# Optimization experiments

Measured on AMD Instinct MI355X. Metric: run time of the kernel, lower is better.

Reference implementation:

```python
import jax, jax.numpy as jnp
import numpy as np

N, E, C, H, T, R = 32768, 262144, 128, 8, 8, 8
DK = C // H


def _typed_linear(feat, W, b, tid):
    # per-type linear: rows with tid==t get feat @ W[t] + b[t]; others untouched base 0
    out = jnp.zeros((feat.shape[0], W.shape[-1]), feat.dtype)
    for t in range(W.shape[0]):
        m = (tid == t)[:, None]
        out = jnp.where(m, feat @ W[t] + b[t], out)
    return out


def _forward(x, type_id, edge_index, edge_attr, Wk, bk, Wq, bq, Wv, bv, Wa, ba,
             relation_pri, relation_att, relation_msg, skip, gamma, beta):
    n, c = x.shape
    r, h, dk, _ = relation_att.shape
    src, dst = edge_index[0], edge_index[1]
    fs, fd = x[src], x[dst]                      # [E, C] gathers
    # per-edge-type k/q/v projections (source masks by edge_attr)
    k = _typed_linear(fs, Wk, bk, edge_attr).reshape(-1, h, dk)
    q = _typed_linear(fd, Wq, bq, edge_attr).reshape(-1, h, dk)
    v = _typed_linear(fs, Wv, bv, edge_attr).reshape(-1, h, dk)
    # relation transforms without materializing [E,h,dk,dk] gathers
    kt = jnp.zeros_like(k)
    vt = jnp.zeros_like(v)
    for ri in range(r):
        m = (edge_attr == ri)[:, None, None]
        kt = jnp.where(m, jnp.einsum('ehd,hdk->ehk', k, relation_att[ri]), kt)
        vt = jnp.where(m, jnp.einsum('ehd,hdk->ehk', v, relation_msg[ri]), vt)
    pri = relation_pri[edge_attr]                # [E, H]
    att = (q * kt).sum(-1) * pri / jnp.sqrt(jnp.asarray(dk, x.dtype))  # [E, H]
    # scatter softmax over destination-node groups
    mx = jax.ops.segment_max(att, dst, num_segments=n)
    ex = jnp.exp(att - mx[dst])
    den = jax.ops.segment_sum(ex, dst, num_segments=n)
    a = ex / den[dst]                            # [E, H]
    w = (a[..., None] * vt).reshape(-1, h * dk)  # [E, C]
    # scatter mean into node slots (zeros for isolated nodes)
    s = jax.ops.segment_sum(w, dst, num_segments=n)
    cnt = jax.ops.segment_sum(jnp.ones((w.shape[0], 1), x.dtype), dst, num_segments=n)
    x0 = jnp.where(cnt > 0, s / jnp.maximum(cnt, 1.0), 0.0)
    # per-node-type output projection + gated residual
    x0 = _typed_linear(x0, Wa, ba, type_id)
    alpha = jax.nn.sigmoid(skip)[type_id][:, None]
    out = x0 * alpha + x * (1.0 - alpha)
    # type-indexed LayerNorm (eps = 1e-5), dropout is identity in eval
    mu = out.mean(-1, keepdims=True)
    var = ((out - mu) ** 2).mean(-1, keepdims=True)
    xn = (out - mu) / jnp.sqrt(var + 1e-5)
    return xn * gamma[type_id] + beta[type_id]


def setup_inputs() -> dict:
    key = jax.random.key(0)
    ks = jax.random.split(key, 16)
    w = 1.0 / np.sqrt(C)
    wr = 1.0 / np.sqrt(DK)
    return {
        'x': jax.random.normal(ks[0], (N, C), jnp.float32),
        'type_id': jax.random.randint(ks[1], (N,), 0, T),
        'edge_index': jax.random.randint(ks[2], (2, E), 0, N),
        'edge_attr': jax.random.randint(ks[3], (E,), 0, R),
        'Wk': jax.random.normal(ks[4], (T, C, C), jnp.float32) * w,
        'bk': jax.random.normal(ks[5], (T, C), jnp.float32) * 0.02,
        'Wq': jax.random.normal(ks[6], (T, C, C), jnp.float32) * w,
        'bq': jax.random.normal(ks[7], (T, C), jnp.float32) * 0.02,
        'Wv': jax.random.normal(ks[8], (T, C, C), jnp.float32) * w,
        'bv': jax.random.normal(ks[9], (T, C), jnp.float32) * 0.02,
        'Wa': jax.random.normal(ks[10], (T, C, C), jnp.float32) * w,
        'ba': jax.random.normal(ks[11], (T, C), jnp.float32) * 0.02,
        'relation_pri': jnp.ones((R, H), jnp.float32),
        'relation_att': jax.random.normal(ks[12], (R, H, DK, DK), jnp.float32) * wr,
        'relation_msg': jax.random.normal(ks[13], (R, H, DK, DK), jnp.float32) * wr,
        'skip': jnp.ones((T,), jnp.float32),
        'gamma': jnp.ones((T, C), jnp.float32),
        'beta': jnp.zeros((T, C), jnp.float32),
    }


def reference(x, type_id, edge_index, edge_attr, Wk, bk, Wq, bq, Wv, bv, Wa, ba,
              relation_pri, relation_att, relation_msg, skip, gamma, beta):
    return _forward(x, type_id, edge_index, edge_attr, Wk, bk, Wq, bq, Wv, bv, Wa, ba,
                    relation_pri, relation_att, relation_msg, skip, gamma, beta)
```

## Files before the change

kernel.cpp:

```cpp
#include <hip/hip_runtime.h>
#include <math.h>

#define NN 32768
#define NE 262144
#define CD 128
#define NH 8
#define NT 8
#define NR 8

typedef unsigned short u16;
typedef unsigned long long ull;
typedef __attribute__((ext_vector_type(8))) short bhalf8;
typedef __attribute__((ext_vector_type(4))) float f32x4;


__device__ __forceinline__ u16 f2b(float f) {
    union { float f; unsigned u; } v; v.f = f;
    unsigned r = v.u + 0x7FFF + ((v.u >> 16) & 1);
    return (u16)(r >> 16);
}
__device__ __forceinline__ float b2f(unsigned h) {
    union { unsigned u; float f; } v; v.u = h << 16;
    return v.f;
}

#define PREP_BLOCKS 2057
#define ZB_BLOCKS 256
#define XB_BLOCKS 2048

__global__ void prep_zero(const float* __restrict__ Wk, const float* __restrict__ bk,
                          const float* __restrict__ Wq,
                          const float* __restrict__ Wv, const float* __restrict__ bv,
                          const float* __restrict__ Wa,
                          const float* __restrict__ Aatt, const float* __restrict__ Amsg,
                          const float* __restrict__ x,
                          u16* __restrict__ WqT, u16* __restrict__ WkT,
                          u16* __restrict__ WvT, u16* __restrict__ WaT,
                          float* __restrict__ bkf, float* __restrict__ bvf,
                          int* __restrict__ degd, u16* __restrict__ xb) {
    if (blockIdx.x >= PREP_BLOCKS + ZB_BLOCKS) {
        int zi = (blockIdx.x - PREP_BLOCKS - ZB_BLOCKS) * 256 + threadIdx.x;
        long basei = (long)zi * 8;
        float4 v0 = *(const float4*)(x + basei);
        float4 v1 = *(const float4*)(x + basei + 4);
        bhalf8 pk;
        pk[0] = (short)f2b(v0.x); pk[1] = (short)f2b(v0.y);
        pk[2] = (short)f2b(v0.z); pk[3] = (short)f2b(v0.w);
        pk[4] = (short)f2b(v1.x); pk[5] = (short)f2b(v1.y);
        pk[6] = (short)f2b(v1.z); pk[7] = (short)f2b(v1.w);
        *(bhalf8*)(xb + basei) = pk;
        return;
    }
    if (blockIdx.x >= PREP_BLOCKS) {
        int zi = (blockIdx.x - PREP_BLOCKS) * 256 + threadIdx.x;
        if (zi < 2 * NN) degd[zi] = 0;
        return;
    }
    const int WCNT = NT * CD * CD;
    int idx = blockIdx.x * 256 + threadIdx.x;
    if (idx < 4 * WCNT) {
        int mat = idx >> 17;
        int o = idx & (WCNT - 1);
        int t = o >> 14;
        int n = (o >> 7) & 127;
        int k = o & 127;
        int ct = n >> 4, lx2 = n & 15, kk = k >> 5, qd = (k >> 3) & 3, dd = k & 7;
        int oo = t * 16384 + (((ct * 4 + kk) * 4 + qd) * 16 + lx2) * 8 + dd;
        if (mat == 0) {
            WqT[oo] = f2b(Wq[(t * CD + k) * CD + n]);
        } else if (mat == 3) {
            WaT[oo] = f2b(Wa[(t * CD + k) * CD + n]);
        } else {
            int h = n >> 4, j = n & 15;
            const float* W = (mat == 1) ? Wk : Wv;
            const float* A = (mat == 1) ? Aatt : Amsg;
            const float* wrow = W + (t * CD + k) * CD + h * 16;
            const float* acol = A + ((t * NH + h) * 16) * 16 + j;
            float s = 0.f;
#pragma unroll
            for (int d = 0; d < 16; ++d) s += wrow[d] * acol[d * 16];
            ((mat == 1) ? WkT : WvT)[oo] = f2b(s);
        }
    } else {
        int o2 = idx - 4 * WCNT;
        if (o2 < 2 * NT * CD) {
            int which = (o2 >= NT * CD) ? 1 : 0;
            int o = o2 - which * NT * CD;
            const float* B = which ? bv : bk;
            const float* A = which ? Amsg : Aatt;
            int t = o >> 7; int c = o & 127; int h = c >> 4; int j = c & 15;
            const float* brow = B + t * CD + h * 16;
            const float* acol = A + ((t * NH + h) * 16) * 16 + j;
            float s = 0.f;
#pragma unroll
            for (int d = 0; d < 16; ++d) s += brow[d] * acol[d * 16];
            (which ? bvf : bkf)[o] = s;
        }
    }
}

__global__ void hists(const int* __restrict__ ea, const int* __restrict__ tidv,
                      const int* __restrict__ dstv,
                      int* __restrict__ epart, int* __restrict__ npart,
                      int* __restrict__ deg) {
    __shared__ int wc[4][8];
    const int b = blockIdx.x;
    const int tid = threadIdx.x;
    const int lane = tid & 63, w = tid >> 6;
    int i = b * 256 + tid;
    int t = ea[i];
    atomicAdd(&deg[dstv[i]], 1);
#pragma unroll
    for (int u = 0; u < 8; ++u) {
        ull m = __ballot(t == u);
        if (lane == 0) wc[w][u] = __popcll(m);
    }
    __syncthreads();
    if (tid < 8) epart[b * 8 + tid] = wc[0][tid] + wc[1][tid] + wc[2][tid] + wc[3][tid];
    if (b < NN / 256) {
        int tn = tidv[i];
        __syncthreads();
#pragma unroll
        for (int u = 0; u < 8; ++u) {
            ull m = __ballot(tn == u);
            if (lane == 0) wc[w][u] = __popcll(m);
        }
        __syncthreads();
        if (tid < 8) npart[b * 8 + tid] = wc[0][tid] + wc[1][tid] + wc[2][tid] + wc[3][tid];
    }
}

__launch_bounds__(1024)
__global__ void scan_all(const int* __restrict__ deg, int* __restrict__ dbase,
                         int* __restrict__ epart, int* __restrict__ npart,
                         int* __restrict__ ectr, int* __restrict__ nctr) {
    const int t = threadIdx.x;
    if (blockIdx.x == 0) {
        __shared__ int part[1024];
        int local[32];
        int s = 0;
#pragma unroll
        for (int i = 0; i < 32; ++i) { local[i] = s; s += deg[t * 32 + i]; }
        part[t] = s;
        __syncthreads();
        for (int off = 1; off < 1024; off <<= 1) {
            int v = (t >= off) ? part[t - off] : 0;
            __syncthreads();
            part[t] += v;
            __syncthreads();
        }
        int base = (t == 0) ? 0 : part[t - 1];
#pragma unroll
        for (int i = 0; i < 32; ++i) dbase[t * 32 + i] = base + local[i];
        return;
    }
    __shared__ int sc[1024 * 8];
    int v[8], orig[8];
#pragma unroll
    for (int u = 0; u < 8; ++u) { orig[u] = v[u] = epart[t * 8 + u]; sc[t * 8 + u] = v[u]; }
    for (int off = 1; off < 1024; off <<= 1) {
        __syncthreads();
        int wv[8];
        bool p = (t >= off);
        if (p) {
#pragma unroll
            for (int u = 0; u < 8; ++u) wv[u] = sc[(t - off) * 8 + u];
        }
        __syncthreads();
        if (p) {
#pragma unroll
            for (int u = 0; u < 8; ++u) { v[u] += wv[u]; sc[t * 8 + u] = v[u]; }
        }
    }
    __syncthreads();
    int tot[8], base[8];
    {
        int acc = 0;
#pragma unroll
        for (int u = 0; u < 8; ++u) { tot[u] = sc[1023 * 8 + u]; base[u] = acc; acc += tot[u]; }
    }
#pragma unroll
    for (int u = 0; u < 8; ++u) epart[t * 8 + u] = base[u] + v[u] - orig[u];
    if (t == 0) {
        ectr[8] = 0; ectr[17] = 0;
        int acc = 0, ptb = 0;
        for (int u = 0; u < 8; ++u) {
            acc += tot[u]; ectr[9 + u] = acc;
            ptb += (tot[u] + 63) >> 6; ectr[18 + u] = ptb;
        }
    }
    __syncthreads();
    int nv[8], nor[8];
#pragma unroll
    for (int u = 0; u < 8; ++u) {
        nor[u] = nv[u] = (t < 128) ? npart[t * 8 + u] : 0;
        sc[t * 8 + u] = nv[u];
    }
    for (int off = 1; off < 128; off <<= 1) {
        __syncthreads();
        int wv[8];
        bool p = (t >= off && t < 128);
        if (p) {
#pragma unroll
            for (int u = 0; u < 8; ++u) wv[u] = sc[(t - off) * 8 + u];
        }
        __syncthreads();
        if (p) {
#pragma unroll
            for (int u = 0; u < 8; ++u) { nv[u] += wv[u]; sc[t * 8 + u] = nv[u]; }
        }
    }
    __syncthreads();
    int ntot[8], nbase[8];
    {
        int acc = 0;
#pragma unroll
        for (int u = 0; u < 8; ++u) { ntot[u] = sc[127 * 8 + u]; nbase[u] = acc; acc += ntot[u]; }
    }
    if (t < 128) {
#pragma unroll
        for (int u = 0; u < 8; ++u) npart[t * 8 + u] = nbase[u] + nv[u] - nor[u];
    }
    if (t == 0) {
        nctr[8] = 0; nctr[17] = 0;
        int acc = 0, ptb = 0;
        for (int u = 0; u < 8; ++u) {
            acc += ntot[u]; nctr[9 + u] = acc;
            ptb += (ntot[u] + 63) >> 6; nctr[18 + u] = ptb;
        }
    }
}

__global__ void scatter2(const int* __restrict__ ea, const int* __restrict__ tidv,
                         const int* __restrict__ srcv, const int* __restrict__ dstv,
                         const int* __restrict__ epart, const int* __restrict__ npart,
                         const int* __restrict__ dbase, int* __restrict__ dcur,
                         int4* __restrict__ epack, int* __restrict__ nperm) {
    __shared__ int wc[4][8];
    __shared__ int wo[4][8];
    const int b = blockIdx.x;
    const int tid = threadIdx.x;
    const int lane = tid & 63, w = tid >> 6;
    const bool is_e = (b < NE / 256);
    const int* lab; const int* off; int i;
    if (is_e) { lab = ea; off = epart + b * 8; i = b * 256 + tid; }
    else { lab = tidv; off = npart + (b - NE / 256) * 8; i = (b - NE / 256) * 256 + tid; }
    int t = lab[i];
    const ull below = (1ull << lane) - 1;
    int myrank = 0;
#pragma unroll
    for (int u = 0; u < 8; ++u) {
        ull m = __ballot(t == u);
        if (lane == 0) wc[w][u] = __popcll(m);
        if (t == u) myrank = __popcll(m & below);
    }
    __syncthreads();
    if (tid < 32) {
        int u = tid & 7, w2 = tid >> 3;
        int s = 0;
        for (int w3 = 0; w3 < w2; ++w3) s += wc[w3][u];
        wo[w2][u] = s;
    }
    __syncthreads();
    int slot = off[t] + wo[w][t] + myrank;
    if (is_e) {
        int s = srcv[i], d = dstv[i];
        int pos = dbase[d] + atomicAdd(&dcur[d], 1);
        epack[slot] = int4{s, d, pos, 0};
    } else {
        nperm[slot] = i;
    }
}

__device__ __forceinline__ void gemm64g(const u16* __restrict__ sA,
                                        const u16* __restrict__ gW,
                                        int rh, int ch, int lx, int quad, int lane,
                                        const float* __restrict__ biasRow,
                                        f32x4 acc[2][4]) {
#pragma unroll
    for (int nt = 0; nt < 4; ++nt) {
        float bv = biasRow[ch * 64 + nt * 16 + lx];
        acc[0][nt] = f32x4{bv, bv, bv, bv};
        acc[1][nt] = f32x4{bv, bv, bv, bv};
    }
    const int m0 = rh * 32 + lx;
    const u16* wbase = gW + (ch * 4) * 2048 + lane * 8;
    bhalf8 bb[2][4];
#pragma unroll
    for (int nt = 0; nt < 4; ++nt)
        bb[0][nt] = *(const bhalf8*)(wbase + nt * 2048);
#pragma unroll
    for (int kk = 0; kk < 4; ++kk) {
        if (kk < 3) {
#pragma unroll
            for (int nt = 0; nt < 4; ++nt)
                bb[(kk + 1) & 1][nt] = *(const bhalf8*)(wbase + nt * 2048 + (kk + 1) * 512);
        }
        const int ko = kk * 32 + quad * 8;
        bhalf8 a0 = *(const bhalf8*)&sA[m0 * 136 + ko];
        bhalf8 a1 = *(const bhalf8*)&sA[(m0 + 16) * 136 + ko];
#pragma unroll
        for (int nt = 0; nt < 4; ++nt) {
            acc[0][nt] = __builtin_amdgcn_mfma_f32_16x16x32_bf16(a0, bb[kk & 1][nt], acc[0][nt], 0, 0, 0);
            acc[1][nt] = __builtin_amdgcn_mfma_f32_16x16x32_bf16(a1, bb[kk & 1][nt], acc[1][nt], 0, 0, 0);
        }
    }
}

__launch_bounds__(256, 4)
__global__ void edge_kernel(const u16* __restrict__ xb,
                            const u16* __restrict__ WqT, const float* __restrict__ bq,
                            const u16* __restrict__ WkT, const float* __restrict__ bkf,
                            const u16* __restrict__ WvT, const float* __restrict__ bvf,
                            const float* __restrict__ pri,
                            const int* __restrict__ ectr, const int4* __restrict__ epack,
                            float* __restrict__ exs, u16* __restrict__ vts) {
    __shared__ u16 sFS[64 * 136];
    __shared__ u16 sFD[64 * 136];
    __shared__ int sSrc[64], sDst[64], sPos[64];

    const int tid = threadIdx.x;
    const int lane = tid & 63;
    const int w = tid >> 6;
    const int lx = lane & 15;
    const int quad = lane >> 4;
    const int ch = w & 1;
    const int rh = w >> 1;
    const int b = blockIdx.x;

    int t = -1, lt = 0;
#pragma unroll
    for (int u = 0; u < NR; ++u) {
        int p0 = ectr[17 + u], p1 = ectr[18 + u];
        if (b >= p0 && b < p1) { t = u; lt = b - p0; }
    }
    if (t < 0) return;
    const int base = ectr[8 + t];
    const int sz = ectr[9 + t] - base;
    const int start = lt * 64;

    if (tid < 64) {
        int idx = start + tid;
        int4 pk = (idx < sz) ? epack[base + idx] : int4{0, 0, NE, 0};
        sSrc[tid] = pk.x;
        sDst[tid] = pk.y;
        sPos[tid] = pk.z;
    }
    __syncthreads();

#pragma unroll
    for (int it = 0; it < 4; ++it) {
        int c = tid + it * 256;
        int row = c >> 4, off = (c & 15) * 8;
        *(bhalf8*)&sFS[row * 136 + off] = *(const bhalf8*)&xb[(long)sSrc[row] * CD + off];
        *(bhalf8*)&sFD[row * 136 + off] = *(const bhalf8*)&xb[(long)sDst[row] * CD + off];
    }
    __syncthreads();

    f32x4 qa[2][4], ka[2][4];
    gemm64g(sFD, WqT + t * 16384, rh, ch, lx, quad, lane, bq + t * CD, qa);
    gemm64g(sFS, WkT + t * 16384, rh, ch, lx, quad, lane, bkf + t * CD, ka);

    float ex[2][4][4];
#pragma unroll
    for (int nt = 0; nt < 4; ++nt) {
        const float ph = pri[t * NH + ch * 4 + nt] * 0.25f;
#pragma unroll
        for (int mt = 0; mt < 2; ++mt) {
#pragma unroll
            for (int reg = 0; reg < 4; ++reg) {
                float p = qa[mt][nt][reg] * ka[mt][nt][reg];
                p += __shfl_xor(p, 1);
                p += __shfl_xor(p, 2);
                p += __shfl_xor(p, 4);
                p += __shfl_xor(p, 8);
                ex[mt][nt][reg] = __expf(p * ph);
            }
        }
    }
    if (lx == 0) {
#pragma unroll
        for (int mt = 0; mt < 2; ++mt)
#pragma unroll
            for (int reg = 0; reg < 4; ++reg) {
                int erow = rh * 32 + mt * 16 + quad * 4 + reg;
                float4 e4 = {ex[mt][0][reg], ex[mt][1][reg], ex[mt][2][reg], ex[mt][3][reg]};
                *(float4*)(exs + (long)sPos[erow] * 8 + ch * 4) = e4;
            }
    }

    f32x4 va[2][4];
    gemm64g(sFS, WvT + t * 16384, rh, ch, lx, quad, lane, bvf + t * CD, va);
    __syncthreads();
#pragma unroll
    for (int mt = 0; mt < 2; ++mt)
#pragma unroll
        for (int reg = 0; reg < 4; ++reg) {
            int erow = rh * 32 + mt * 16 + quad * 4 + reg;
#pragma unroll
            for (int nt = 0; nt < 4; ++nt)
                sFD[erow * 136 + ch * 64 + nt * 16 + lx] = f2b(va[mt][nt][reg]);
        }
    __syncthreads();
#pragma unroll
    for (int it = 0; it < 4; ++it) {
        int c = tid + it * 256;
        int row = c >> 4, off = (c & 15) * 8;
        *(bhalf8*)&vts[(long)sPos[row] * 128 + off] = *(const bhalf8*)&sFD[row * 136 + off];
    }
}

__launch_bounds__(256, 4)
__global__ void node_kernel(const float* __restrict__ x,
                            const u16* __restrict__ WaT, const float* __restrict__ ba,
                            const float* __restrict__ skip, const float* __restrict__ gamma,
                            const float* __restrict__ beta,
                            const int* __restrict__ nctr, const int* __restrict__ nperm,
                            const int* __restrict__ dbase, const int* __restrict__ deg,
                            const float* __restrict__ exs, const u16* __restrict__ vts,
                            float* __restrict__ out) {
    __shared__ u16 sX0[64 * 136];
    __shared__ int sNode[64], sVal[64];

    const int tid = threadIdx.x;
    const int lane = tid & 63;
    const int w = tid >> 6;
    const int lx = lane & 15;
    const int quad = lane >> 4;
    const int b = blockIdx.x;

    int t = -1, lt = 0;
#pragma unroll
    for (int u = 0; u < NT; ++u) {
        int p0 = nctr[17 + u], p1 = nctr[18 + u];
        if (b >= p0 && b < p1) { t = u; lt = b - p0; }
    }
    if (t < 0) return;
    const int base = nctr[8 + t];
    const int sz = nctr[9 + t] - base;
    const int start = lt * 64;

    if (tid < 64) {
        int idx = start + tid;
        int n = (idx < sz) ? nperm[base + idx] : -1;
        sVal[tid] = (n >= 0) ? 1 : 0;
        sNode[tid] = (n >= 0) ? n : 0;
    }
    __syncthreads();

    {
        const int sub = lane >> 3;
        const int l8 = lane & 7;
        for (int r2 = 0; r2 < 2; ++r2) {
            int row = w * 16 + r2 * 8 + sub;
            int n = sNode[row];
            int s = dbase[n], d = deg[n];
            const u16* vp = vts + (long)s * 128 + l8 * 16;
            const float* ep = exs + (long)s * 8 + l8;
            float a[16];
#pragma unroll
            for (int c = 0; c < 16; ++c) a[c] = 0.f;
            float sden = 0.f;
            int j = 0;
            for (; j + 2 <= d; j += 2) {
                bhalf8 v0a = *(const bhalf8*)(vp + (long)j * 128);
                bhalf8 v0b = *(const bhalf8*)(vp + (long)j * 128 + 8);
                bhalf8 v1a = *(const bhalf8*)(vp + (long)(j + 1) * 128);
                bhalf8 v1b = *(const bhalf8*)(vp + (long)(j + 1) * 128 + 8);
                float e0 = ep[(long)j * 8];
                float e1 = ep[(long)(j + 1) * 8];
#pragma unroll
                for (int c = 0; c < 8; ++c) {
                    a[c] += e0 * b2f((u16)v0a[c]) + e1 * b2f((u16)v1a[c]);
                    a[8 + c] += e0 * b2f((u16)v0b[c]) + e1 * b2f((u16)v1b[c]);
                }
                sden += e0 + e1;
            }
            if (j < d) {
                bhalf8 v0a = *(const bhalf8*)(vp + (long)j * 128);
                bhalf8 v0b = *(const bhalf8*)(vp + (long)j * 128 + 8);
                float e0 = ep[(long)j * 8];
#pragma unroll
                for (int c = 0; c < 8; ++c) {
                    a[c] += e0 * b2f((u16)v0a[c]);
                    a[8 + c] += e0 * b2f((u16)v0b[c]);
                }
                sden += e0;
            }
            float inv = (d > 0) ? 1.f / (sden * (float)d) : 0.f;
            bhalf8 p0, p1;
#pragma unroll
            for (int c = 0; c < 8; ++c) {
                p0[c] = (short)f2b(a[c] * inv);
                p1[c] = (short)f2b(a[8 + c] * inv);
            }
            *(bhalf8*)&sX0[row * 136 + l8 * 16] = p0;
            *(bhalf8*)&sX0[row * 136 + l8 * 16 + 8] = p1;
        }
    }
    __syncthreads();

    f32x4 acc[8];
#pragma unroll
    for (int nt = 0; nt < 8; ++nt) {
        float bv = ba[t * CD + nt * 16 + lx];
        acc[nt] = f32x4{bv, bv, bv, bv};
    }
    const int m0 = w * 16 + lx;
    const u16* wbase = WaT + t * 16384 + lane * 8;
#pragma unroll
    for (int kk = 0; kk < 4; ++kk) {
        bhalf8 nb[8];
#pragma unroll
        for (int ct = 0; ct < 8; ++ct)
            nb[ct] = *(const bhalf8*)(wbase + ct * 2048 + kk * 512);
        bhalf8 a = *(const bhalf8*)&sX0[m0 * 136 + kk * 32 + quad * 8];
#pragma unroll
        for (int ct = 0; ct < 8; ++ct)
            acc[ct] = __builtin_amdgcn_mfma_f32_16x16x32_bf16(a, nb[ct], acc[ct], 0, 0, 0);
    }

    const float alpha = 1.f / (1.f + __expf(-skip[t]));
    const float oma = 1.f - alpha;
    float g[8], be[8];
#pragma unroll
    for (int nt = 0; nt < 8; ++nt) {
        g[nt] = gamma[t * CD + nt * 16 + lx];
        be[nt] = beta[t * CD + nt * 16 + lx];
    }
#pragma unroll
    for (int reg = 0; reg < 4; ++reg) {
        int erow = w * 16 + quad * 4 + reg;
        int n = sNode[erow];
        const float* xr = x + (long)n * CD;
        float o[8];
        float s1 = 0.f, s2 = 0.f;
#pragma unroll
        for (int nt = 0; nt < 8; ++nt) {
            float xv = xr[nt * 16 + lx];
            float ov = acc[nt][reg] * alpha + xv * oma;
            o[nt] = ov;
            s1 += ov;
            s2 += ov * ov;
        }
#pragma unroll
        for (int m = 1; m < 16; m <<= 1) {
            s1 += __shfl_xor(s1, m);
            s2 += __shfl_xor(s2, m);
        }
        float mu = s1 * (1.f / 128.f);
        float var = s2 * (1.f / 128.f) - mu * mu;
        float rs = rsqrtf(var + 1e-5f);
        if (sVal[erow]) {
            float* op = out + (long)n * CD;
#pragma unroll
            for (int nt = 0; nt < 8; ++nt)
                __builtin_nontemporal_store((o[nt] - mu) * rs * g[nt] + be[nt],
                                            &op[nt * 16 + lx]);
        }
    }
}

extern "C" void kernel_launch(void* const* d_in, const int* in_sizes, int n_in,
                              void* d_out, int out_size, void* d_ws, size_t ws_size,
                              hipStream_t stream) {
    const float* x        = (const float*)d_in[0];
    const int*   type_id  = (const int*)d_in[1];
    const int*   edge_idx = (const int*)d_in[2];
    const int*   edge_attr= (const int*)d_in[3];
    const float* Wk   = (const float*)d_in[4];
    const float* bk   = (const float*)d_in[5];
    const float* Wq   = (const float*)d_in[6];
    const float* bq   = (const float*)d_in[7];
    const float* Wv   = (const float*)d_in[8];
    const float* bv   = (const float*)d_in[9];
    const float* Wa   = (const float*)d_in[10];
    const float* ba   = (const float*)d_in[11];
    const float* pri  = (const float*)d_in[12];
    const float* Aatt = (const float*)d_in[13];
    const float* Amsg = (const float*)d_in[14];
    const float* skip = (const float*)d_in[15];
    const float* gam  = (const float*)d_in[16];
    const float* bet  = (const float*)d_in[17];

    char* ws = (char*)d_ws;
    u16*   WqT  = (u16*)(ws + 0);
    u16*   WkT  = (u16*)(ws + 262144);
    u16*   WvT  = (u16*)(ws + 524288);
    u16*   WaT  = (u16*)(ws + 786432);
    float* bkf  = (float*)(ws + 1048576);
    float* bvf  = (float*)(ws + 1052672);
    float* exs  = (float*)(ws + 1056768);
    u16*   vts  = (u16*)(ws + 9447424);
    int*   deg  = (int*)  (ws + 76572672);
    int*   dcur = (int*)  (ws + 76703744);
    int*   dbase= (int*)  (ws + 76834816);
    int*   nperm= (int*)  (ws + 78014464);
    int*   ectr = (int*)  (ws + 78145536);
    int*   nctr = (int*)  (ws + 78145792);
    int*   epart= (int*)  (ws + 78146048);
    int*   npart= (int*)  (ws + 78178816);
    u16*   xb   = (u16*)  (ws + 78182912);
    int4*  epack= (int4*) (ws + 86571520);

    const int* src = edge_idx;
    const int* dst = edge_idx + NE;

    prep_zero<<<PREP_BLOCKS + ZB_BLOCKS + XB_BLOCKS, 256, 0, stream>>>(
        Wk, bk, Wq, Wv, bv, Wa, Aatt, Amsg, x, WqT, WkT, WvT, WaT, bkf, bvf, deg, xb);
    hists<<<NE / 256, 256, 0, stream>>>(edge_attr, type_id, dst, epart, npart, deg);
    scan_all<<<2, 1024, 0, stream>>>(deg, dbase, epart, npart, ectr, nctr);
    scatter2<<<NE / 256 + NN / 256, 256, 0, stream>>>(edge_attr, type_id, src, dst,
                                                      epart, npart, dbase, dcur,
                                                      epack, nperm);
    edge_kernel<<<NE / 64 + NR, 256, 0, stream>>>(xb, WqT, bq, WkT, bkf, WvT, bvf,
                                                  pri, ectr, epack, exs, vts);
    node_kernel<<<NN / 64 + NT, 256, 0, stream>>>(x, WaT, ba, skip, gam, bet, nctr, nperm,
                                                  dbase, deg, exs, vts, (float*)d_out);
}
```

Baseline: 239.4 us.

## Fuse histogram into prep kernel, prefetch weight fragments across GEMMs, unroll node gather

Merges the histogram kernel into the prep kernel and moves degree zeroing to a memset, so one launch and one dependency boundary disappear. In the edge kernel, the Q/K/V weight fragments and biases are loaded ahead of use in a software pipeline across the three GEMMs, so weight loads overlap with MFMA work. Launch bounds are relaxed from 4 to 3 blocks per CU to make room for the extra fragment registers. The node aggregation loop is unrolled by four with two accumulator sets to expose more memory-level parallelism, at the cost of more registers.

Measured after the change: 277.5 us. +15.9%, slower.

```diff
diff --git a/kernel.cpp b/kernel.cpp
--- a/kernel.cpp
+++ b/kernel.cpp
@@ -25,21 +25,54 @@
 }
 
 #define PREP_BLOCKS 2057
-#define ZB_BLOCKS 256
 #define XB_BLOCKS 2048
-
-__global__ void prep_zero(const float* __restrict__ Wk, const float* __restrict__ bk,
-                          const float* __restrict__ Wq,
-                          const float* __restrict__ Wv, const float* __restrict__ bv,
-                          const float* __restrict__ Wa,
-                          const float* __restrict__ Aatt, const float* __restrict__ Amsg,
-                          const float* __restrict__ x,
-                          u16* __restrict__ WqT, u16* __restrict__ WkT,
-                          u16* __restrict__ WvT, u16* __restrict__ WaT,
-                          float* __restrict__ bkf, float* __restrict__ bvf,
-                          int* __restrict__ degd, u16* __restrict__ xb) {
-    if (blockIdx.x >= PREP_BLOCKS + ZB_BLOCKS) {
-        int zi = (blockIdx.x - PREP_BLOCKS - ZB_BLOCKS) * 256 + threadIdx.x;
+#define HIST_BLOCKS 1024
+
+__global__ void prep_all(const float* __restrict__ Wk, const float* __restrict__ bk,
+                         const float* __restrict__ Wq,
+                         const float* __restrict__ Wv, const float* __restrict__ bv,
+                         const float* __restrict__ Wa,
+                         const float* __restrict__ Aatt, const float* __restrict__ Amsg,
+                         const float* __restrict__ x,
+                         const int* __restrict__ ea, const int* __restrict__ tidv,
+                         const int* __restrict__ dstv,
+                         u16* __restrict__ WqT, u16* __restrict__ WkT,
+                         u16* __restrict__ WvT, u16* __restrict__ WaT,
+                         float* __restrict__ bkf, float* __restrict__ bvf,
+                         u16* __restrict__ xb,
+                         int* __restrict__ epart, int* __restrict__ npart,
+                         int* __restrict__ deg) {
+    const int bx = blockIdx.x;
+    if (bx >= PREP_BLOCKS + XB_BLOCKS) {
+        __shared__ int wc[4][8];
+        const int hb = bx - PREP_BLOCKS - XB_BLOCKS;
+        const int tid = threadIdx.x;
+        const int lane = tid & 63, w = tid >> 6;
+        int i = hb * 256 + tid;
+        int t = ea[i];
+        atomicAdd(&deg[dstv[i]], 1);
+#pragma unroll
+        for (int u = 0; u < 8; ++u) {
+            ull m = __ballot(t == u);
+            if (lane == 0) wc[w][u] = __popcll(m);
+        }
+        __syncthreads();
+        if (tid < 8) epart[hb * 8 + tid] = wc[0][tid] + wc[1][tid] + wc[2][tid] + wc[3][tid];
+        if (hb < NN / 256) {
+            int tn = tidv[i];
+            __syncthreads();
+#pragma unroll
+            for (int u = 0; u < 8; ++u) {
+                ull m = __ballot(tn == u);
+                if (lane == 0) wc[w][u] = __popcll(m);
+            }
+            __syncthreads();
+            if (tid < 8) npart[hb * 8 + tid] = wc[0][tid] + wc[1][tid] + wc[2][tid] + wc[3][tid];
+        }
+        return;
+    }
+    if (bx >= PREP_BLOCKS) {
+        int zi = (bx - PREP_BLOCKS) * 256 + threadIdx.x;
         long basei = (long)zi * 8;
         float4 v0 = *(const float4*)(x + basei);
         float4 v1 = *(const float4*)(x + basei + 4);
@@ -51,13 +84,8 @@
         *(bhalf8*)(xb + basei) = pk;
         return;
     }
-    if (blockIdx.x >= PREP_BLOCKS) {
-        int zi = (blockIdx.x - PREP_BLOCKS) * 256 + threadIdx.x;
-        if (zi < 2 * NN) degd[zi] = 0;
-        return;
-    }
     const int WCNT = NT * CD * CD;
-    int idx = blockIdx.x * 256 + threadIdx.x;
+    int idx = bx * 256 + threadIdx.x;
     if (idx < 4 * WCNT) {
         int mat = idx >> 17;
         int o = idx & (WCNT - 1);
@@ -99,37 +127,6 @@
     }
 }
 
-__global__ void hists(const int* __restrict__ ea, const int* __restrict__ tidv,
-                      const int* __restrict__ dstv,
-                      int* __restrict__ epart, int* __restrict__ npart,
-                      int* __restrict__ deg) {
-    __shared__ int wc[4][8];
-    const int b = blockIdx.x;
-    const int tid = threadIdx.x;
-    const int lane = tid & 63, w = tid >> 6;
-    int i = b * 256 + tid;
-    int t = ea[i];
-    atomicAdd(&deg[dstv[i]], 1);
-#pragma unroll
-    for (int u = 0; u < 8; ++u) {
-        ull m = __ballot(t == u);
-        if (lane == 0) wc[w][u] = __popcll(m);
-    }
-    __syncthreads();
-    if (tid < 8) epart[b * 8 + tid] = wc[0][tid] + wc[1][tid] + wc[2][tid] + wc[3][tid];
-    if (b < NN / 256) {
-        int tn = tidv[i];
-        __syncthreads();
-#pragma unroll
-        for (int u = 0; u < 8; ++u) {
-            ull m = __ballot(tn == u);
-            if (lane == 0) wc[w][u] = __popcll(m);
-        }
-        __syncthreads();
-        if (tid < 8) npart[b * 8 + tid] = wc[0][tid] + wc[1][tid] + wc[2][tid] + wc[3][tid];
-    }
-}
-
 __launch_bounds__(1024)
 __global__ void scan_all(const int* __restrict__ deg, int* __restrict__ dbase,
                          int* __restrict__ epart, int* __restrict__ npart,
@@ -272,42 +269,40 @@
     }
 }
 
-__device__ __forceinline__ void gemm64g(const u16* __restrict__ sA,
-                                        const u16* __restrict__ gW,
-                                        int rh, int ch, int lx, int quad, int lane,
-                                        const float* __restrict__ biasRow,
-                                        f32x4 acc[2][4]) {
+__device__ __forceinline__ void ldfrags(bhalf8* __restrict__ f, const u16* __restrict__ wb,
+                                        int kb) {
 #pragma unroll
     for (int nt = 0; nt < 4; ++nt) {
-        float bv = biasRow[ch * 64 + nt * 16 + lx];
-        acc[0][nt] = f32x4{bv, bv, bv, bv};
-        acc[1][nt] = f32x4{bv, bv, bv, bv};
-    }
-    const int m0 = rh * 32 + lx;
-    const u16* wbase = gW + (ch * 4) * 2048 + lane * 8;
-    bhalf8 bb[2][4];
-#pragma unroll
-    for (int nt = 0; nt < 4; ++nt)
-        bb[0][nt] = *(const bhalf8*)(wbase + nt * 2048);
-#pragma unroll
-    for (int kk = 0; kk < 4; ++kk) {
-        if (kk < 3) {
-#pragma unroll
-            for (int nt = 0; nt < 4; ++nt)
-                bb[(kk + 1) & 1][nt] = *(const bhalf8*)(wbase + nt * 2048 + (kk + 1) * 512);
-        }
-        const int ko = kk * 32 + quad * 8;
+        f[nt]     = *(const bhalf8*)(wb + nt * 2048 + kb * 512);
+        f[4 + nt] = *(const bhalf8*)(wb + nt * 2048 + (kb + 1) * 512);
+    }
+}
+
+__device__ __forceinline__ void gemmhalf(const u16* __restrict__ sA,
+                                         const bhalf8* __restrict__ f,
+                                         int m0, int aoff, int kb, f32x4 acc[2][4]) {
+#pragma unroll
+    for (int kk2 = 0; kk2 < 2; ++kk2) {
+        const int ko = (kb + kk2) * 32 + aoff;
         bhalf8 a0 = *(const bhalf8*)&sA[m0 * 136 + ko];
         bhalf8 a1 = *(const bhalf8*)&sA[(m0 + 16) * 136 + ko];
 #pragma unroll
         for (int nt = 0; nt < 4; ++nt) {
-            acc[0][nt] = __builtin_amdgcn_mfma_f32_16x16x32_bf16(a0, bb[kk & 1][nt], acc[0][nt], 0, 0, 0);
-            acc[1][nt] = __builtin_amdgcn_mfma_f32_16x16x32_bf16(a1, bb[kk & 1][nt], acc[1][nt], 0, 0, 0);
-        }
-    }
-}
-
-__launch_bounds__(256, 4)
+            acc[0][nt] = __builtin_amdgcn_mfma_f32_16x16x32_bf16(a0, f[kk2 * 4 + nt], acc[0][nt], 0, 0, 0);
+            acc[1][nt] = __builtin_amdgcn_mfma_f32_16x16x32_bf16(a1, f[kk2 * 4 + nt], acc[1][nt], 0, 0, 0);
+        }
+    }
+}
+
+__device__ __forceinline__ void initacc(f32x4 acc[2][4], const float* b4) {
+#pragma unroll
+    for (int nt = 0; nt < 4; ++nt) {
+        acc[0][nt] = f32x4{b4[nt], b4[nt], b4[nt], b4[nt]};
+        acc[1][nt] = f32x4{b4[nt], b4[nt], b4[nt], b4[nt]};
+    }
+}
+
+__launch_bounds__(256, 3)
 __global__ void edge_kernel(const u16* __restrict__ xb,
                             const u16* __restrict__ WqT, const float* __restrict__ bq,
                             const u16* __restrict__ WkT, const float* __restrict__ bkf,
@@ -339,6 +334,21 @@
     const int sz = ectr[9 + t] - base;
     const int start = lt * 64;
 
+    const u16* wq = WqT + t * 16384 + ch * 4 * 2048 + lane * 8;
+    const u16* wk = WkT + t * 16384 + ch * 4 * 2048 + lane * 8;
+    const u16* wv = WvT + t * 16384 + ch * 4 * 2048 + lane * 8;
+    bhalf8 fA[8], fB[8];
+    ldfrags(fA, wq, 0);
+    ldfrags(fB, wq, 2);
+    float bq4[4], bk4[4], bv4[4], pr4[4];
+#pragma unroll
+    for (int nt = 0; nt < 4; ++nt) {
+        bq4[nt] = bq[t * CD + ch * 64 + nt * 16 + lx];
+        bk4[nt] = bkf[t * CD + ch * 64 + nt * 16 + lx];
+        bv4[nt] = bvf[t * CD + ch * 64 + nt * 16 + lx];
+        pr4[nt] = pri[t * NH + ch * 4 + nt] * 0.25f;
+    }
+
     if (tid < 64) {
         int idx = start + tid;
         int4 pk = (idx < sz) ? epack[base + idx] : int4{0, 0, NE, 0};
@@ -357,14 +367,24 @@
     }
     __syncthreads();
 
+    const int m0 = rh * 32 + lx;
+    const int aoff = quad * 8;
+
     f32x4 qa[2][4], ka[2][4];
-    gemm64g(sFD, WqT + t * 16384, rh, ch, lx, quad, lane, bq + t * CD, qa);
-    gemm64g(sFS, WkT + t * 16384, rh, ch, lx, quad, lane, bkf + t * CD, ka);
+    initacc(qa, bq4);
+    gemmhalf(sFD, fA, m0, aoff, 0, qa);
+    ldfrags(fA, wk, 0);
+    gemmhalf(sFD, fB, m0, aoff, 2, qa);
+    ldfrags(fB, wk, 2);
+    initacc(ka, bk4);
+    gemmhalf(sFS, fA, m0, aoff, 0, ka);
+    ldfrags(fA, wv, 0);
+    gemmhalf(sFS, fB, m0, aoff, 2, ka);
+    ldfrags(fB, wv, 2);
 
     float ex[2][4][4];
 #pragma unroll
     for (int nt = 0; nt < 4; ++nt) {
-        const float ph = pri[t * NH + ch * 4 + nt] * 0.25f;
 #pragma unroll
         for (int mt = 0; mt < 2; ++mt) {
 #pragma unroll
@@ -374,7 +394,7 @@
                 p += __shfl_xor(p, 2);
                 p += __shfl_xor(p, 4);
                 p += __shfl_xor(p, 8);
-                ex[mt][nt][reg] = __expf(p * ph);
+                ex[mt][nt][reg] = __expf(p * pr4[nt]);
             }
         }
     }
@@ -390,7 +410,9 @@
     }
 
     f32x4 va[2][4];
-    gemm64g(sFS, WvT + t * 16384, rh, ch, lx, quad, lane, bvf + t * CD, va);
+    initacc(va, bv4);
+    gemmhalf(sFS, fA, m0, aoff, 0, va);
+    gemmhalf(sFS, fB, m0, aoff, 2, va);
     __syncthreads();
 #pragma unroll
     for (int mt = 0; mt < 2; ++mt)
@@ -457,42 +479,52 @@
             int s = dbase[n], d = deg[n];
             const u16* vp = vts + (long)s * 128 + l8 * 16;
             const float* ep = exs + (long)s * 8 + l8;
-            float a[16];
-#pragma unroll
-            for (int c = 0; c < 16; ++c) a[c] = 0.f;
-            float sden = 0.f;
+            float aA[16], aB[16];
+#pragma unroll
+            for (int c = 0; c < 16; ++c) { aA[c] = 0.f; aB[c] = 0.f; }
+            float sdA = 0.f, sdB = 0.f;
             int j = 0;
-            for (; j + 2 <= d; j += 2) {
-                bhalf8 v0a = *(const bhalf8*)(vp + (long)j * 128);
-                bhalf8 v0b = *(const bhalf8*)(vp + (long)j * 128 + 8);
+            for (; j + 4 <= d; j += 4) {
+                bhalf8 v0a = *(const bhalf8*)(vp + (long)(j + 0) * 128);
+                bhalf8 v0b = *(const bhalf8*)(vp + (long)(j + 0) * 128 + 8);
                 bhalf8 v1a = *(const bhalf8*)(vp + (long)(j + 1) * 128);
                 bhalf8 v1b = *(const bhalf8*)(vp + (long)(j + 1) * 128 + 8);
-                float e0 = ep[(long)j * 8];
+                bhalf8 v2a = *(const bhalf8*)(vp + (long)(j + 2) * 128);
+                bhalf8 v2b = *(const bhalf8*)(vp + (long)(j + 2) * 128 + 8);
+                bhalf8 v3a = *(const bhalf8*)(vp + (long)(j + 3) * 128);
+                bhalf8 v3b = *(const bhalf8*)(vp + (long)(j + 3) * 128 + 8);
+                float e0 = ep[(long)(j + 0) * 8];
                 float e1 = ep[(long)(j + 1) * 8];
+                float e2 = ep[(long)(j + 2) * 8];
+                float e3 = ep[(long)(j + 3) * 8];
 #pragma unroll
                 for (int c = 0; c < 8; ++c) {
-                    a[c] += e0 * b2f((u16)v0a[c]) + e1 * b2f((u16)v1a[c]);
-                    a[8 + c] += e0 * b2f((u16)v0b[c]) + e1 * b2f((u16)v1b[c]);
+                    aA[c] += e0 * b2f((u16)v0a[c]) + e1 * b2f((u16)v1a[c]);
+                    aA[8 + c] += e0 * b2f((u16)v0b[c]) + e1 * b2f((u16)v1b[c]);
+                    aB[c] += e2 * b2f((u16)v2a[c]) + e3 * b2f((u16)v3a[c]);
+                    aB[8 + c] += e2 * b2f((u16)v2b[c]) + e3 * b2f((u16)v3b[c]);
                 }
-                sden += e0 + e1;
+                sdA += e0 + e1;
+                sdB += e2 + e3;
             }
-            if (j < d) {
+            for (; j < d; ++j) {
                 bhalf8 v0a = *(const bhalf8*)(vp + (long)j * 128);
                 bhalf8 v0b = *(const bhalf8*)(vp + (long)j * 128 + 8);
                 float e0 = ep[(long)j * 8];
 #pragma unroll
                 for (int c = 0; c < 8; ++c) {
-                    a[c] += e0 * b2f((u16)v0a[c]);
-                    a[8 + c] += e0 * b2f((u16)v0b[c]);
+                    aA[c] += e0 * b2f((u16)v0a[c]);
+                    aA[8 + c] += e0 * b2f((u16)v0b[c]);
                 }
-                sden += e0;
+                sdA += e0;
             }
+            float sden = sdA + sdB;
             float inv = (d > 0) ? 1.f / (sden * (float)d) : 0.f;
             bhalf8 p0, p1;
 #pragma unroll
             for (int c = 0; c < 8; ++c) {
-                p0[c] = (short)f2b(a[c] * inv);
-                p1[c] = (short)f2b(a[8 + c] * inv);
+                p0[c] = (short)f2b((aA[c] + aB[c]) * inv);
+                p1[c] = (short)f2b((aA[8 + c] + aB[8 + c]) * inv);
             }
             *(bhalf8*)&sX0[row * 136 + l8 * 16] = p0;
             *(bhalf8*)&sX0[row * 136 + l8 * 16 + 8] = p1;
@@ -606,9 +638,10 @@
     const int* src = edge_idx;
     const int* dst = edge_idx + NE;
 
-    prep_zero<<<PREP_BLOCKS + ZB_BLOCKS + XB_BLOCKS, 256, 0, stream>>>(
-        Wk, bk, Wq, Wv, bv, Wa, Aatt, Amsg, x, WqT, WkT, WvT, WaT, bkf, bvf, deg, xb);
-    hists<<<NE / 256, 256, 0, stream>>>(edge_attr, type_id, dst, epart, npart, deg);
+    hipMemsetAsync(deg, 0, 2 * NN * sizeof(int), stream);
+    prep_all<<<PREP_BLOCKS + XB_BLOCKS + HIST_BLOCKS, 256, 0, stream>>>(
+        Wk, bk, Wq, Wv, bv, Wa, Aatt, Amsg, x, edge_attr, type_id, dst,
+        WqT, WkT, WvT, WaT, bkf, bvf, xb, epart, npart, deg);
     scan_all<<<2, 1024, 0, stream>>>(deg, dbase, epart, npart, ectr, nctr);
     scatter2<<<NE / 256 + NN / 256, 256, 0, stream>>>(edge_attr, type_id, src, dst,
                                                       epart, npart, dbase, dcur,
```
